# Performance work log

Hardware: AMD Instinct MI355X
Metric: run time of the kernel (lower is better)

The kernel has to match this reference:

```python
import jax, jax.numpy as jnp
import numpy as np

TEMPERATURE = 0.5


def setup_inputs() -> dict:
    key = jax.random.key(0)
    k1, k2 = jax.random.split(key)
    N, D = 4096, 512
    emb_i = jax.random.normal(k1, (N, D), dtype=jnp.float32)
    emb_j = jax.random.normal(k2, (N, D), dtype=jnp.float32)
    return {"emb_i": emb_i, "emb_j": emb_j}


def reference(emb_i, emb_j):
    # L2-normalize each embedding row (F.normalize, dim=1)
    z_i = emb_i / jnp.linalg.norm(emb_i, axis=1, keepdims=True)
    z_j = emb_j / jnp.linalg.norm(emb_j, axis=1, keepdims=True)
    reps = jnp.concatenate([z_i, z_j], axis=0)  # [2N, D]
    N = emb_i.shape[0]
    M = 2 * N
    # cosine similarity of normalized vectors == dot product -> [2N, 2N]
    sim = jnp.einsum('id,jd->ij', reps, reps) / TEMPERATURE
    # denominator: sum_k!=i exp(sim[i,k]); original multiplies by one-hot complement
    exp_sim = jnp.exp(sim)
    denom = jnp.sum(exp_sim, axis=1) - jnp.diagonal(exp_sim)  # [2N]
    log_denom = jnp.log(denom)
    # positive pairs: (k, k+N) and (k+N, k)
    idx = jnp.arange(N)
    pos_ij = sim[idx, idx + N]          # sim(k, k+N)/T
    pos_ji = sim[idx + N, idx]          # sim(k+N, k)/T
    loss = jnp.sum(-(pos_ij - log_denom[:N]) - (pos_ji - log_denom[N:]))
    return loss / (2.0 * N)
```

## Files before the change

### kernel.cpp

```cpp
#include <hip/hip_runtime.h>
#include <cstdint>
#include <cstddef>

constexpr int N_ROWS = 4096;
constexpr int D      = 512;
constexpr int M      = 8192;
constexpr int NTILE  = 64;
constexpr int NBLK   = NTILE * (NTILE + 1) / 2;
constexpr int LDSOFF = 128 * 32;

using f32x4  = __attribute__((ext_vector_type(4))) float;
using bf16x8 = __attribute__((ext_vector_type(8))) __bf16;
using us8    = __attribute__((ext_vector_type(8))) unsigned short;

__device__ inline unsigned short f2bf(float f) {
    unsigned int u = __float_as_uint(f);
    u += 0x7fffu + ((u >> 16) & 1u);
    return (unsigned short)(u >> 16);
}
__device__ inline float bf2f(unsigned short s) {
    return __uint_as_float(((unsigned int)s) << 16);
}

#define ASYNC_CP16(gsrc, ldst)                                                      \
    __builtin_amdgcn_global_load_lds(                                               \
        (const __attribute__((address_space(1))) unsigned int*)(gsrc),              \
        (__attribute__((address_space(3))) unsigned int*)(ldst), 16, 0, 0)

__global__ __launch_bounds__(256) void normpos_kernel(
    const float* __restrict__ emb_i, const float* __restrict__ emb_j,
    unsigned short* __restrict__ zb, float* __restrict__ diagss,
    float* __restrict__ pos)
{
    const int wave = threadIdx.x >> 6, lane = threadIdx.x & 63;
    const int k = blockIdx.x * 4 + wave;

    const float4* a = (const float4*)(emb_i + (size_t)k * D);
    const float4* b = (const float4*)(emb_j + (size_t)k * D);
    float4 a0 = a[lane * 2], a1 = a[lane * 2 + 1];
    float4 b0 = b[lane * 2], b1 = b[lane * 2 + 1];

    float ssi = a0.x*a0.x + a0.y*a0.y + a0.z*a0.z + a0.w*a0.w
              + a1.x*a1.x + a1.y*a1.y + a1.z*a1.z + a1.w*a1.w;
    float ssj = b0.x*b0.x + b0.y*b0.y + b0.z*b0.z + b0.w*b0.w
              + b1.x*b1.x + b1.y*b1.y + b1.z*b1.z + b1.w*b1.w;
    float dp  = a0.x*b0.x + a0.y*b0.y + a0.z*b0.z + a0.w*b0.w
              + a1.x*b1.x + a1.y*b1.y + a1.z*b1.z + a1.w*b1.w;
    #pragma unroll
    for (int off = 32; off; off >>= 1) {
        ssi += __shfl_xor(ssi, off, 64);
        ssj += __shfl_xor(ssj, off, 64);
        dp  += __shfl_xor(dp,  off, 64);
    }
    const float invi = rsqrtf(ssi), invj = rsqrtf(ssj);

    const float zi[8] = {a0.x*invi, a0.y*invi, a0.z*invi, a0.w*invi,
                         a1.x*invi, a1.y*invi, a1.z*invi, a1.w*invi};
    const float zj[8] = {b0.x*invj, b0.y*invj, b0.z*invj, b0.w*invj,
                         b1.x*invj, b1.y*invj, b1.z*invj, b1.w*invj};
    us8 pi, pj;
    float dssi = 0.f, dssj = 0.f;
    #pragma unroll
    for (int t = 0; t < 8; ++t) {
        unsigned short bi = f2bf(zi[t]), bj = f2bf(zj[t]);
        pi[t] = bi; pj[t] = bj;
        float fi = bf2f(bi), fj = bf2f(bj);
        dssi += fi * fi; dssj += fj * fj;
    }
    *(us8*)(zb + (size_t)k * D + lane * 8)            = pi;
    *(us8*)(zb + (size_t)(k + N_ROWS) * D + lane * 8) = pj;
    #pragma unroll
    for (int off = 32; off; off >>= 1) {
        dssi += __shfl_xor(dssi, off, 64);
        dssj += __shfl_xor(dssj, off, 64);
    }
    if (lane == 0) {
        diagss[k]          = dssi;
        diagss[k + N_ROWS] = dssj;
        pos[k]             = 2.0f * dp * invi * invj;
    }
}

__global__ __launch_bounds__(256, 4) void simgemm_kernel(
    const unsigned short* __restrict__ zb, float* __restrict__ partials)
{
    __shared__ unsigned short As[2 * 128 * 32];
    __shared__ unsigned short Bs[2 * 128 * 32];
    __shared__ float rp[4][64];
    __shared__ float cp4[4][64];
    const int tid  = threadIdx.x;
    const int wave = tid >> 6, lane = tid & 63;
    const int l15  = lane & 15, ks = lane >> 4;

    const int t = blockIdx.x;
    int bi = (int)((129.0f - sqrtf(129.0f * 129.0f - 8.0f * (float)t)) * 0.5f);
    while (bi > 0 && bi * (129 - bi) / 2 > t) --bi;
    while ((bi + 1) * (129 - (bi + 1)) / 2 <= t) ++bi;
    const int bj = bi + (t - bi * (129 - bi) / 2);
    const bool diag = (bi == bj);

    const int wrow = (wave >> 1) * 64, wcol = (wave & 1) * 64;

    const int ch0 = wave * 2;
    const int sr0 = ch0 * 16 + (lane >> 2);
    const int sc  = ((lane & 3) ^ ((sr0 >> 1) & 3)) * 8;
    const unsigned short* gA0 = zb + (size_t)(bi * 128 + sr0) * D + sc;
    const unsigned short* gB0 = zb + (size_t)(bj * 128 + sr0) * D + sc;
    unsigned short* lA = As + ch0 * 512;
    unsigned short* lB = Bs + ch0 * 512;

    ASYNC_CP16(gA0,          lA);
    ASYNC_CP16(gA0 + 16 * D, lA + 512);
    ASYNC_CP16(gB0,          lB);
    ASYNC_CP16(gB0 + 16 * D, lB + 512);

    f32x4 acc[4][4] = {};
    const int swOff = (ks ^ ((l15 >> 1) & 3)) * 8;

    #pragma unroll 2
    for (int it = 0; it < D / 32; ++it) {
        __syncthreads();

        if (it + 1 < D / 32) {
            const int kc  = (it + 1) * 32;
            const int off = ((it + 1) & 1) * LDSOFF;
            ASYNC_CP16(gA0 + kc,          lA + off);
            ASYNC_CP16(gA0 + kc + 16 * D, lA + off + 512);
            ASYNC_CP16(gB0 + kc,          lB + off);
            ASYNC_CP16(gB0 + kc + 16 * D, lB + off + 512);
        }

        const int cb = (it & 1) * LDSOFF;
        bf16x8 af[4], bg[4];
        #pragma unroll
        for (int f = 0; f < 4; ++f) {
            af[f] = *(const bf16x8*)(As + cb + (wrow + f * 16 + l15) * 32 + swOff);
            bg[f] = *(const bf16x8*)(Bs + cb + (wcol + f * 16 + l15) * 32 + swOff);
        }
        #pragma unroll
        for (int i = 0; i < 4; ++i)
            #pragma unroll
            for (int j = 0; j < 4; ++j)
                acc[i][j] = __builtin_amdgcn_mfma_f32_16x16x32_bf16(
                    af[i], bg[j], acc[i][j], 0, 0, 0);
    }

    float rowp[4][4] = {};
    #pragma unroll
    for (int j = 0; j < 4; ++j) {
        float cpj = 0.f;
        #pragma unroll
        for (int i = 0; i < 4; ++i)
            #pragma unroll
            for (int r = 0; r < 4; ++r) {
                float e = __expf(2.0f * acc[i][j][r]);
                rowp[i][r] += e;
                cpj += e;
            }
        if (!diag) {
            cpj += __shfl_xor(cpj, 16, 64);
            cpj += __shfl_xor(cpj, 32, 64);
            if (ks == 0) cp4[wave][j * 16 + l15] = cpj;
        }
    }
    #pragma unroll
    for (int i = 0; i < 4; ++i)
        #pragma unroll
        for (int r = 0; r < 4; ++r) {
            float e = rowp[i][r];
            e += __shfl_xor(e, 1, 64);
            e += __shfl_xor(e, 2, 64);
            e += __shfl_xor(e, 4, 64);
            e += __shfl_xor(e, 8, 64);
            if (l15 == 0) rp[wave][i * 16 + ks * 4 + r] = e;
        }
    __syncthreads();

    float* pA = partials + (size_t)(bi * NTILE + bj) * 128;
    float* pB = partials + (size_t)(bj * NTILE + bi) * 128;
    if (tid < 128) {
        const int h = tid >> 6, rr = tid & 63;
        pA[tid] = rp[h * 2][rr] + rp[h * 2 + 1][rr];
    } else if (!diag) {
        const int c = tid - 128, h = c >> 6, cc = c & 63;
        pB[c] = cp4[h][cc] + cp4[h + 2][cc];
    }
}

__global__ __launch_bounds__(256) void rowfin_kernel(
    const float* __restrict__ partials, const float* __restrict__ diagss,
    const float* __restrict__ pos, float* __restrict__ lgpart)
{
    const int r  = blockIdx.x;
    const int ri = threadIdx.x & 127;
    const int ch = threadIdx.x >> 7;
    const float* base = partials + (size_t)r * NTILE * 128 + ri;
    float s = 0.f;
    #pragma unroll
    for (int c = 0; c < 32; ++c)
        s += base[(size_t)(ch * 32 + c) * 128];
    __shared__ float half1[128];
    __shared__ float red[4];
    if (ch == 1) half1[ri] = s;
    __syncthreads();
    float lg = 0.f;
    if (ch == 0) {
        float rs = s + half1[ri];
        int row = r * 128 + ri;
        lg = __logf(rs - __expf(2.0f * diagss[row]));
    }
    if (threadIdx.x < 64)
        lg -= 2.0f * pos[r * 64 + threadIdx.x];
    #pragma unroll
    for (int off = 32; off; off >>= 1) lg += __shfl_xor(lg, off, 64);
    const int wave = threadIdx.x >> 6, lane = threadIdx.x & 63;
    if (lane == 0) red[wave] = lg;
    __syncthreads();
    if (threadIdx.x == 0) lgpart[r] = red[0] + red[1] + red[2] + red[3];
}

__global__ __launch_bounds__(64) void loss_kernel(
    const float* __restrict__ lgpart, float* __restrict__ out)
{
    float local = lgpart[threadIdx.x];
    #pragma unroll
    for (int off = 32; off; off >>= 1) local += __shfl_xor(local, off, 64);
    if (threadIdx.x == 0) out[0] = local * (1.0f / 8192.0f);
}

extern "C" void kernel_launch(void* const* d_in, const int* in_sizes, int n_in,
                              void* d_out, int out_size, void* d_ws, size_t ws_size,
                              hipStream_t stream)
{
    const float* emb_i = (const float*)d_in[0];
    const float* emb_j = (const float*)d_in[1];

    unsigned short* zb = (unsigned short*)d_ws;
    float* partials = (float*)((char*)d_ws + (size_t)M * D * sizeof(unsigned short));
    float* diagss   = partials + (size_t)NTILE * NTILE * 128;
    float* pos      = diagss + M;
    float* lgpart   = pos + N_ROWS;
    float* out      = (float*)d_out;

    normpos_kernel<<<N_ROWS / 4, 256, 0, stream>>>(emb_i, emb_j, zb, diagss, pos);
    simgemm_kernel<<<NBLK, 256, 0, stream>>>(zb, partials);
    rowfin_kernel<<<NTILE, 256, 0, stream>>>(partials, diagss, pos, lgpart);
    loss_kernel<<<1, 64, 0, stream>>>(lgpart, out);
}
```

Measured before the change: 122.4 us.

## Switch similarity GEMM from bf16 to fp8 MFMA with permuted row layout

```diff
diff --git a/kernel.cpp b/kernel.cpp
--- a/kernel.cpp
+++ b/kernel.cpp
@@ -7,29 +7,29 @@
 constexpr int M      = 8192;
 constexpr int NTILE  = 64;
 constexpr int NBLK   = NTILE * (NTILE + 1) / 2;
-constexpr int LDSOFF = 128 * 32;
-
-using f32x4  = __attribute__((ext_vector_type(4))) float;
-using bf16x8 = __attribute__((ext_vector_type(8))) __bf16;
-using us8    = __attribute__((ext_vector_type(8))) unsigned short;
-
-__device__ inline unsigned short f2bf(float f) {
-    unsigned int u = __float_as_uint(f);
-    u += 0x7fffu + ((u >> 16) & 1u);
-    return (unsigned short)(u >> 16);
-}
-__device__ inline float bf2f(unsigned short s) {
-    return __uint_as_float(((unsigned int)s) << 16);
-}
+constexpr int BKB    = 64;
+constexpr int LDSB   = 128 * BKB;
+
+using f32x4 = __attribute__((ext_vector_type(4))) float;
+using ul2   = __attribute__((ext_vector_type(2))) unsigned long;
 
 #define ASYNC_CP16(gsrc, ldst)                                                      \
     __builtin_amdgcn_global_load_lds(                                               \
         (const __attribute__((address_space(1))) unsigned int*)(gsrc),              \
         (__attribute__((address_space(3))) unsigned int*)(ldst), 16, 0, 0)
 
+#define SS_FP8(pk, accum)                                                           \
+    do {                                                                            \
+        float f0 = __builtin_amdgcn_cvt_f32_fp8((pk), 0);                           \
+        float f1 = __builtin_amdgcn_cvt_f32_fp8((pk), 1);                           \
+        float f2 = __builtin_amdgcn_cvt_f32_fp8((pk), 2);                           \
+        float f3 = __builtin_amdgcn_cvt_f32_fp8((pk), 3);                           \
+        (accum) += f0 * f0 + f1 * f1 + f2 * f2 + f3 * f3;                           \
+    } while (0)
+
 __global__ __launch_bounds__(256) void normpos_kernel(
     const float* __restrict__ emb_i, const float* __restrict__ emb_j,
-    unsigned short* __restrict__ zb, float* __restrict__ diagss,
+    uint8_t* __restrict__ zb, float* __restrict__ diagss,
     float* __restrict__ pos)
 {
     const int wave = threadIdx.x >> 6, lane = threadIdx.x & 63;
@@ -58,17 +58,31 @@
                          a1.x*invi, a1.y*invi, a1.z*invi, a1.w*invi};
     const float zj[8] = {b0.x*invj, b0.y*invj, b0.z*invj, b0.w*invj,
                          b1.x*invj, b1.y*invj, b1.z*invj, b1.w*invj};
-    us8 pi, pj;
+
+    int pi0 = __builtin_amdgcn_cvt_pk_fp8_f32(zi[0], zi[1], 0, false);
+    pi0     = __builtin_amdgcn_cvt_pk_fp8_f32(zi[2], zi[3], pi0, true);
+    int pi1 = __builtin_amdgcn_cvt_pk_fp8_f32(zi[4], zi[5], 0, false);
+    pi1     = __builtin_amdgcn_cvt_pk_fp8_f32(zi[6], zi[7], pi1, true);
+    int pj0 = __builtin_amdgcn_cvt_pk_fp8_f32(zj[0], zj[1], 0, false);
+    pj0     = __builtin_amdgcn_cvt_pk_fp8_f32(zj[2], zj[3], pj0, true);
+    int pj1 = __builtin_amdgcn_cvt_pk_fp8_f32(zj[4], zj[5], 0, false);
+    pj1     = __builtin_amdgcn_cvt_pk_fp8_f32(zj[6], zj[7], pj1, true);
+
     float dssi = 0.f, dssj = 0.f;
-    #pragma unroll
-    for (int t = 0; t < 8; ++t) {
-        unsigned short bi = f2bf(zi[t]), bj = f2bf(zj[t]);
-        pi[t] = bi; pj[t] = bj;
-        float fi = bf2f(bi), fj = bf2f(bj);
-        dssi += fi * fi; dssj += fj * fj;
-    }
-    *(us8*)(zb + (size_t)k * D + lane * 8)            = pi;
-    *(us8*)(zb + (size_t)(k + N_ROWS) * D + lane * 8) = pj;
+    SS_FP8(pi0, dssi);
+    SS_FP8(pi1, dssi);
+    SS_FP8(pj0, dssj);
+    SS_FP8(pj1, dssj);
+
+    const int g = lane, bb = g >> 3, w = g & 7;
+    const int sl = bb * 8 + ((w < 4) ? (w * 2) : ((w - 4) * 2 + 1));
+    const unsigned long long vi =
+        ((unsigned long long)(unsigned)pi1 << 32) | (unsigned)pi0;
+    const unsigned long long vj =
+        ((unsigned long long)(unsigned)pj1 << 32) | (unsigned)pj0;
+    *(unsigned long long*)(zb + (size_t)k * D + sl * 8)            = vi;
+    *(unsigned long long*)(zb + (size_t)(k + N_ROWS) * D + sl * 8) = vj;
+
     #pragma unroll
     for (int off = 32; off; off >>= 1) {
         dssi += __shfl_xor(dssi, off, 64);
@@ -82,12 +96,15 @@
 }
 
 __global__ __launch_bounds__(256, 4) void simgemm_kernel(
-    const unsigned short* __restrict__ zb, float* __restrict__ partials)
-{
-    __shared__ unsigned short As[2 * 128 * 32];
-    __shared__ unsigned short Bs[2 * 128 * 32];
+    const uint8_t* __restrict__ zb, float* __restrict__ partials)
+{
+    __shared__ ul2 AsV[2 * LDSB / 16];
+    __shared__ ul2 BsV[2 * LDSB / 16];
     __shared__ float rp[4][64];
     __shared__ float cp4[4][64];
+    uint8_t* As = (uint8_t*)AsV;
+    uint8_t* Bs = (uint8_t*)BsV;
+
     const int tid  = threadIdx.x;
     const int wave = tid >> 6, lane = tid & 63;
     const int l15  = lane & 15, ks = lane >> 4;
@@ -101,48 +118,49 @@
 
     const int wrow = (wave >> 1) * 64, wcol = (wave & 1) * 64;
 
-    const int ch0 = wave * 2;
-    const int sr0 = ch0 * 16 + (lane >> 2);
-    const int sc  = ((lane & 3) ^ ((sr0 >> 1) & 3)) * 8;
-    const unsigned short* gA0 = zb + (size_t)(bi * 128 + sr0) * D + sc;
-    const unsigned short* gB0 = zb + (size_t)(bj * 128 + sr0) * D + sc;
-    unsigned short* lA = As + ch0 * 512;
-    unsigned short* lB = Bs + ch0 * 512;
-
-    ASYNC_CP16(gA0,          lA);
-    ASYNC_CP16(gA0 + 16 * D, lA + 512);
-    ASYNC_CP16(gB0,          lB);
-    ASYNC_CP16(gB0 + 16 * D, lB + 512);
+    const int srow = wave * 32 + (lane >> 2);
+    const int scol = ((lane & 3) ^ ((lane >> 3) & 3)) * 16;
+    const uint8_t* gA = zb + (size_t)(bi * 128 + srow) * D + scol;
+    const uint8_t* gB = zb + (size_t)(bj * 128 + srow) * D + scol;
+    uint8_t* lA = As + wave * 32 * BKB;
+    uint8_t* lB = Bs + wave * 32 * BKB;
+
+    ASYNC_CP16(gA,            lA);
+    ASYNC_CP16(gA + 16 * D,   lA + 16 * BKB);
+    ASYNC_CP16(gB,            lB);
+    ASYNC_CP16(gB + 16 * D,   lB + 16 * BKB);
 
     f32x4 acc[4][4] = {};
-    const int swOff = (ks ^ ((l15 >> 1) & 3)) * 8;
-
-    #pragma unroll 2
-    for (int it = 0; it < D / 32; ++it) {
+    const int swb = (ks ^ ((l15 >> 1) & 3)) * 16;
+
+    for (int it = 0; it < D / BKB; ++it) {
         __syncthreads();
 
-        if (it + 1 < D / 32) {
-            const int kc  = (it + 1) * 32;
-            const int off = ((it + 1) & 1) * LDSOFF;
-            ASYNC_CP16(gA0 + kc,          lA + off);
-            ASYNC_CP16(gA0 + kc + 16 * D, lA + off + 512);
-            ASYNC_CP16(gB0 + kc,          lB + off);
-            ASYNC_CP16(gB0 + kc + 16 * D, lB + off + 512);
-        }
-
-        const int cb = (it & 1) * LDSOFF;
-        bf16x8 af[4], bg[4];
+        if (it + 1 < D / BKB) {
+            const int kc  = (it + 1) * BKB;
+            const int off = ((it + 1) & 1) * LDSB;
+            ASYNC_CP16(gA + kc,          lA + off);
+            ASYNC_CP16(gA + kc + 16 * D, lA + off + 16 * BKB);
+            ASYNC_CP16(gB + kc,          lB + off);
+            ASYNC_CP16(gB + kc + 16 * D, lB + off + 16 * BKB);
+        }
+
+        const int cb = (it & 1) * LDSB;
+        ul2 af[4], bg[4];
         #pragma unroll
         for (int f = 0; f < 4; ++f) {
-            af[f] = *(const bf16x8*)(As + cb + (wrow + f * 16 + l15) * 32 + swOff);
-            bg[f] = *(const bf16x8*)(Bs + cb + (wcol + f * 16 + l15) * 32 + swOff);
+            af[f] = *(const ul2*)(As + cb + (wrow + f * 16 + l15) * BKB + swb);
+            bg[f] = *(const ul2*)(Bs + cb + (wcol + f * 16 + l15) * BKB + swb);
         }
         #pragma unroll
         for (int i = 0; i < 4; ++i)
             #pragma unroll
-            for (int j = 0; j < 4; ++j)
-                acc[i][j] = __builtin_amdgcn_mfma_f32_16x16x32_bf16(
-                    af[i], bg[j], acc[i][j], 0, 0, 0);
+            for (int j = 0; j < 4; ++j) {
+                acc[i][j] = __builtin_amdgcn_mfma_f32_16x16x32_fp8_fp8(
+                    (long)af[i][0], (long)bg[j][0], acc[i][j], 0, 0, 0);
+                acc[i][j] = __builtin_amdgcn_mfma_f32_16x16x32_fp8_fp8(
+                    (long)af[i][1], (long)bg[j][1], acc[i][j], 0, 0, 0);
+            }
     }
 
     float rowp[4][4] = {};
@@ -235,8 +253,8 @@
     const float* emb_i = (const float*)d_in[0];
     const float* emb_j = (const float*)d_in[1];
 
-    unsigned short* zb = (unsigned short*)d_ws;
-    float* partials = (float*)((char*)d_ws + (size_t)M * D * sizeof(unsigned short));
+    uint8_t* zb = (uint8_t*)d_ws;
+    float* partials = (float*)((char*)d_ws + (size_t)M * D);
     float* diagss   = partials + (size_t)NTILE * NTILE * 128;
     float* pos      = diagss + M;
     float* lgpart   = pos + N_ROWS;
```

Result: faster. 103.6 us (-15.3%).
